# Optimization experiments

Hardware: AMD Instinct MI355X
Metric: run time of the kernel (lower is better)

## Reference

```python
import jax, jax.numpy as jnp
import numpy as np

B, C, H, W = 32, 256, 32, 32
D = max(16, C // 4)  # 64
K = 8


def setup_inputs() -> dict:
    key = jax.random.key(0)
    ks = jax.random.split(key, 4)
    x = jax.random.normal(ks[0], (B, C, H, W), dtype=jnp.float32)
    wq = jax.random.normal(ks[1], (D, C), dtype=jnp.float32) * (1.0 / np.sqrt(C))
    wk = jax.random.normal(ks[2], (D, C), dtype=jnp.float32) * (1.0 / np.sqrt(C))
    wv = jax.random.normal(ks[3], (C, C), dtype=jnp.float32) * (1.0 / np.sqrt(C))
    bq = jnp.zeros((D,), dtype=jnp.float32)
    bk = jnp.zeros((D,), dtype=jnp.float32)
    bv = jnp.zeros((C,), dtype=jnp.float32)
    scale = jnp.ones((1,), dtype=jnp.float32)
    return {"x": x, "wq": wq, "bq": bq, "wk": wk, "bk": bk, "wv": wv, "bv": bv, "scale": scale}


def reference(x, wq, bq, wk, bk, wv, bv, scale):
    b, c, h, w = x.shape
    n = h * w
    xf = x.reshape(b, c, n)                      # [B,C,N]
    # 1x1 convs are pointwise GEMMs over the channel dim
    q = jnp.einsum('dc,bcn->bdn', wq, xf) + bq[None, :, None]   # [B,D,N]
    k = jnp.einsum('dc,bcn->bdn', wk, xf) + bk[None, :, None]   # [B,D,N]
    v = jnp.einsum('ec,bcn->ben', wv, xf) + bv[None, :, None]   # [B,C,N]
    d = q.shape[1]
    sim = jnp.einsum('bdn,bdm->bnm', q, k) / jnp.sqrt(jnp.float32(d))  # [B,N,N]
    sim = sim - 1e9 * jnp.eye(n, dtype=sim.dtype)[None]          # mask self
    topk_val, topk_idx = jax.lax.top_k(sim, K)                    # [B,N,K]
    weights = jax.nn.softmax(topk_val, axis=-1)                   # [B,N,K]
    v_t = v.transpose(0, 2, 1)                                    # [B,N,C]
    gathered = v_t[jnp.arange(b)[:, None, None], topk_idx]        # [B,N,K,C]
    out = jnp.einsum('bnk,bnkc->bnc', weights, gathered)          # [B,N,C]
    out = out.transpose(0, 2, 1).reshape(b, c, h, w)
    return x + scale * out
```

## Files before the change

### kernel.cpp

```cpp
#include <hip/hip_runtime.h>
#include <hip/hip_bf16.h>

#define B_ 32
#define C_ 256
#define N_ 1024
#define D_ 64

typedef __attribute__((ext_vector_type(8))) short bf16x8;
typedef __attribute__((ext_vector_type(4))) float f32x4;

__device__ __forceinline__ unsigned long long pack_key(float v, int m) {
    const unsigned int bits = __float_as_uint(v);
    const unsigned int mono = (bits & 0x80000000u) ? ~bits : (bits | 0x80000000u);
    return ((unsigned long long)mono << 10) | (unsigned long long)(1023 - m);
}

template <int CTRL>
__device__ __forceinline__ float dpp_mov_f(float x) {
    return __int_as_float(__builtin_amdgcn_update_dpp(
        0, __float_as_int(x), CTRL, 0xF, 0xF, true));
}
#define DPP_QUAD_XOR1   0xB1
#define DPP_QUAD_XOR2   0x4E
#define DPP_HALF_MIRROR 0x141
#define DPP_ROW_ROR8    0x128

template <int CTRL>
__device__ __forceinline__ unsigned long long dpp_max_u64(unsigned long long k) {
    const unsigned int lo = (unsigned int)k;
    const unsigned int hi = (unsigned int)(k >> 32);
    const unsigned int plo = (unsigned int)__builtin_amdgcn_update_dpp(0, (int)lo, CTRL, 0xF, 0xF, true);
    const unsigned int phi = (unsigned int)__builtin_amdgcn_update_dpp(0, (int)hi, CTRL, 0xF, 0xF, true);
    const unsigned long long p = ((unsigned long long)phi << 32) | plo;
    return p > k ? p : k;
}

__device__ __forceinline__ unsigned short f2bf(float f) {
    __hip_bfloat16 h = __float2bfloat16(f);
    return *(unsigned short*)&h;
}

__global__ __launch_bounds__(256) void prep_kernel(
    const float* __restrict__ x,
    const float* __restrict__ wq, const float* __restrict__ wk,
    const float* __restrict__ wv, float* __restrict__ wt,
    unsigned short* __restrict__ wvb, unsigned short* __restrict__ xtb,
    int mfma_path)
{
    __shared__ __align__(16) float tl[64][65];
    const int bid = blockIdx.x;
    const int t = threadIdx.x;

    if (bid < 256) {
        const int c = bid;
        for (int r = t; r < 384; r += 256) {
            float v;
            if      (r < 64)  v = wq[(size_t)r * C_ + c];
            else if (r < 128) v = wk[(size_t)(r - 64) * C_ + c];
            else              v = wv[(size_t)(r - 128) * C_ + c];
            wt[(size_t)c * 384 + r] = v;
        }
        if (mfma_path) wvb[(size_t)c * C_ + t] = f2bf(wv[(size_t)c * C_ + t]);
        return;
    }
    if (!mfma_path) return;

    const int lid = bid - 256;
    const int b     = (lid & 7) + 8 * (lid >> 9);
    const int inner = (lid >> 3) & 63;
    const int nt    = inner & 15;
    const int ct    = inner >> 4;
    const int n0 = nt * 64, c0 = ct * 64;

    const float* xb = x + (size_t)b * C_ * N_;
    #pragma unroll
    for (int p = 0; p < 4; ++p) {
        const int cl = (t >> 4) + p * 16;
        const int nl = (t & 15) * 4;
        *(float4*)&tl[cl][nl] = *(const float4*)&xb[(size_t)(c0 + cl) * N_ + n0 + nl];
    }
    __syncthreads();

    unsigned short* dstb = xtb + ((size_t)b * N_) * C_;
    #pragma unroll
    for (int p = 0; p < 4; ++p) {
        const int nl = (t >> 4) + p * 16;
        const int cl = (t & 15) * 4;
        ushort4 o;
        o.x = f2bf(tl[cl + 0][nl]);
        o.y = f2bf(tl[cl + 1][nl]);
        o.z = f2bf(tl[cl + 2][nl]);
        o.w = f2bf(tl[cl + 3][nl]);
        *(ushort4*)&dstb[(size_t)(n0 + nl) * C_ + c0 + cl] = o;
    }
}

__global__ __launch_bounds__(256) void projfused_kernel(
    const float* __restrict__ x, const float* __restrict__ wt,
    const float* __restrict__ bq, const float* __restrict__ bk,
    float* __restrict__ qk,
    const unsigned short* __restrict__ xtb, const unsigned short* __restrict__ wvb,
    const float* __restrict__ bv, float* __restrict__ vt)
{
    const int bid = blockIdx.x;
    const int t = threadIdx.x;
    const int lane = t & 63;

    if (bid < 1024) {
        const int lid = bid;
        const int b     = (lid & 7) + 8 * (lid >> 8);
        const int inner = (lid >> 3) & 31;
        const int rg    = inner & 7;
        const int nt    = inner >> 3;
        const int r0 = rg * 16;
        const int n0 = nt * 256;
        const int wu = __builtin_amdgcn_readfirstlane(t >> 6);
        const int rw = r0 + wu * 4;

        float acc[4][4];
        #pragma unroll
        for (int i = 0; i < 4; ++i)
            #pragma unroll
            for (int j = 0; j < 4; ++j) acc[i][j] = 0.f;

        const float* xp = x + (size_t)b * C_ * N_ + n0 + lane * 4;
        const float* wp = wt + rw;

        #pragma unroll 8
        for (int c = 0; c < C_; ++c) {
            const float4 xv = *(const float4*)(xp + (size_t)c * N_);
            const float4 w0 = *(const float4*)(wp + (size_t)c * 384);
            const float wv4[4] = { w0.x, w0.y, w0.z, w0.w };
            #pragma unroll
            for (int i = 0; i < 4; ++i) {
                acc[i][0] = fmaf(wv4[i], xv.x, acc[i][0]);
                acc[i][1] = fmaf(wv4[i], xv.y, acc[i][1]);
                acc[i][2] = fmaf(wv4[i], xv.z, acc[i][2]);
                acc[i][3] = fmaf(wv4[i], xv.w, acc[i][3]);
            }
        }

        #pragma unroll
        for (int i = 0; i < 4; ++i) {
            const int R = rw + i;
            const float bb = (R < 64) ? bq[R] : bk[R - 64];
            float4 o; o.x = acc[i][0]+bb; o.y = acc[i][1]+bb; o.z = acc[i][2]+bb; o.w = acc[i][3]+bb;
            *(float4*)&qk[((size_t)b * 128 + R) * N_ + n0 + lane * 4] = o;
        }
    } else {
        const int lid = bid - 1024;
        const int b     = (lid & 7) + 8 * (lid >> 9);
        const int inner = (lid >> 3) & 63;
        const int nb    = inner & 15;
        const int eb    = inner >> 4;
        const int w  = t >> 6;
        const int n_base = nb * 64 + (w & 1) * 32;
        const int e_base = eb * 64 + (w >> 1) * 32;

        const int l16  = lane & 15;
        const int koff = 8 * (lane >> 4);

        f32x4 acc[2][2];
        #pragma unroll
        for (int i = 0; i < 2; ++i)
            #pragma unroll
            for (int j = 0; j < 2; ++j) acc[i][j] = (f32x4)(0.f);

        const unsigned short* ab = wvb + (size_t)(e_base + l16) * C_ + koff;
        const unsigned short* bb = xtb + ((size_t)b * N_ + n_base + l16) * C_ + koff;

        #pragma unroll
        for (int kk = 0; kk < 8; ++kk) {
            const int c0 = kk * 32;
            bf16x8 a0 = *(const bf16x8*)(ab + c0);
            bf16x8 a1 = *(const bf16x8*)(ab + 16 * C_ + c0);
            bf16x8 b0 = *(const bf16x8*)(bb + c0);
            bf16x8 b1 = *(const bf16x8*)(bb + 16 * C_ + c0);
            acc[0][0] = __builtin_amdgcn_mfma_f32_16x16x32_bf16(a0, b0, acc[0][0], 0, 0, 0);
            acc[0][1] = __builtin_amdgcn_mfma_f32_16x16x32_bf16(a0, b1, acc[0][1], 0, 0, 0);
            acc[1][0] = __builtin_amdgcn_mfma_f32_16x16x32_bf16(a1, b0, acc[1][0], 0, 0, 0);
            acc[1][1] = __builtin_amdgcn_mfma_f32_16x16x32_bf16(a1, b1, acc[1][1], 0, 0, 0);
        }

        const int col  = lane & 15;
        const int row0 = (lane >> 4) * 4;
        #pragma unroll
        for (int i = 0; i < 2; ++i) {
            const int e0 = e_base + i * 16 + row0;
            const float4 bvv = *(const float4*)&bv[e0];
            #pragma unroll
            for (int j = 0; j < 2; ++j) {
                const int n = n_base + j * 16 + col;
                float4 o;
                o.x = acc[i][j][0] + bvv.x; o.y = acc[i][j][1] + bvv.y;
                o.z = acc[i][j][2] + bvv.z; o.w = acc[i][j][3] + bvv.w;
                *(float4*)&vt[((size_t)b * N_ + n) * C_ + e0] = o;
            }
        }
    }
}

__global__ __launch_bounds__(256) void proj_full_kernel(
    const float* __restrict__ x, const float* __restrict__ wt,
    const float* __restrict__ bq, const float* __restrict__ bk,
    const float* __restrict__ bv,
    float* __restrict__ qk, float* __restrict__ vt)
{
    const int lid = blockIdx.x;
    const int b     = (lid & 7) + 8 * (lid / 384);
    const int inner = (lid >> 3) % 48;
    const int rg    = inner % 12;
    const int nt    = inner / 12;
    const int r0 = rg * 32;
    const int n0 = nt * 256;
    const int lane = threadIdx.x & 63;
    const int wu = __builtin_amdgcn_readfirstlane(threadIdx.x >> 6);
    const int rw = r0 + wu * 8;

    float acc[8][4];
    #pragma unroll
    for (int i = 0; i < 8; ++i)
        #pragma unroll
        for (int j = 0; j < 4; ++j) acc[i][j] = 0.f;

    const float* xp = x + (size_t)b * C_ * N_ + n0 + lane * 4;
    const float* wp = wt + rw;

    #pragma unroll 8
    for (int c = 0; c < C_; ++c) {
        const float4 xv = *(const float4*)(xp + (size_t)c * N_);
        const float* wr = wp + (size_t)c * 384;
        const float4 w0 = *(const float4*)(wr);
        const float4 w1 = *(const float4*)(wr + 4);
        const float wv8[8] = { w0.x, w0.y, w0.z, w0.w, w1.x, w1.y, w1.z, w1.w };
        #pragma unroll
        for (int i = 0; i < 8; ++i) {
            acc[i][0] = fmaf(wv8[i], xv.x, acc[i][0]);
            acc[i][1] = fmaf(wv8[i], xv.y, acc[i][1]);
            acc[i][2] = fmaf(wv8[i], xv.z, acc[i][2]);
            acc[i][3] = fmaf(wv8[i], xv.w, acc[i][3]);
        }
    }

    if (r0 < 128) {
        #pragma unroll
        for (int i = 0; i < 8; ++i) {
            const int R = rw + i;
            const float bb = (R < 64) ? bq[R] : bk[R - 64];
            float4 o; o.x = acc[i][0]+bb; o.y = acc[i][1]+bb; o.z = acc[i][2]+bb; o.w = acc[i][3]+bb;
            *(float4*)&qk[((size_t)b * 128 + R) * N_ + n0 + lane * 4] = o;
        }
    } else {
        const int e0 = rw - 128;
        float be[8];
        #pragma unroll
        for (int i = 0; i < 8; ++i) be[i] = bv[e0 + i];
        #pragma unroll
        for (int j = 0; j < 4; ++j) {
            const int n = n0 + lane * 4 + j;
            float* dst = &vt[((size_t)b * N_ + n) * C_ + e0];
            float4 o0; o0.x = acc[0][j]+be[0]; o0.y = acc[1][j]+be[1]; o0.z = acc[2][j]+be[2]; o0.w = acc[3][j]+be[3];
            float4 o1; o1.x = acc[4][j]+be[4]; o1.y = acc[5][j]+be[5]; o1.z = acc[6][j]+be[6]; o1.w = acc[7][j]+be[7];
            *(float4*)dst       = o0;
            *(float4*)(dst + 4) = o1;
        }
    }
}

__global__ __launch_bounds__(512) void attn_kernel(
    const float* __restrict__ x,
    const float* __restrict__ qk,
    const float* __restrict__ vt,
    const float* __restrict__ scale,
    float* __restrict__ out)
{
    const int lid = blockIdx.x;
    const int b  = (lid & 7) + 8 * (lid >> 9);
    const int n0 = ((lid >> 3) & 63) * 16;
    const int t  = threadIdx.x;
    const int lane = t & 63;
    const int w  = t >> 6;
    const int ms = w & 3;
    const int rg = __builtin_amdgcn_readfirstlane(t >> 8);

    __shared__ unsigned long long cand[16][196];
    __shared__ int   ccnt[16][4];

    const int m_base = ms * 256 + lane * 4;

    float a0[8], a1[8], a2[8], a3[8];
    #pragma unroll
    for (int r = 0; r < 8; ++r) { a0[r]=0.f; a1[r]=0.f; a2[r]=0.f; a3[r]=0.f; }

    const float* kb = qk + ((size_t)b * 128 + 64) * N_ + m_base;
    const float* qb = qk + (size_t)b * 128 * N_ + n0 + rg * 8;

    #pragma unroll 2
    for (int d0 = 0; d0 < D_; d0 += 4) {
        const float4 k0 = *(const float4*)&kb[(size_t)(d0+0) * N_];
        const float4 k1 = *(const float4*)&kb[(size_t)(d0+1) * N_];
        const float4 k2 = *(const float4*)&kb[(size_t)(d0+2) * N_];
        const float4 k3 = *(const float4*)&kb[(size_t)(d0+3) * N_];

        float qs[4][8];
        #pragma unroll
        for (int dd = 0; dd < 4; ++dd) {
            #pragma unroll
            for (int rq = 0; rq < 2; ++rq) {
                const float4 qv = *(const float4*)&qb[(size_t)(d0 + dd) * N_ + rq * 4];
                qs[dd][rq*4+0] = qv.x; qs[dd][rq*4+1] = qv.y;
                qs[dd][rq*4+2] = qv.z; qs[dd][rq*4+3] = qv.w;
            }
        }

        #pragma unroll
        for (int r = 0; r < 8; ++r) {
            a0[r] = fmaf(qs[0][r], k0.x, a0[r]); a0[r] = fmaf(qs[1][r], k1.x, a0[r]);
            a0[r] = fmaf(qs[2][r], k2.x, a0[r]); a0[r] = fmaf(qs[3][r], k3.x, a0[r]);
            a1[r] = fmaf(qs[0][r], k0.y, a1[r]); a1[r] = fmaf(qs[1][r], k1.y, a1[r]);
            a1[r] = fmaf(qs[2][r], k2.y, a1[r]); a1[r] = fmaf(qs[3][r], k3.y, a1[r]);
            a2[r] = fmaf(qs[0][r], k0.z, a2[r]); a2[r] = fmaf(qs[1][r], k1.z, a2[r]);
            a2[r] = fmaf(qs[2][r], k2.z, a2[r]); a2[r] = fmaf(qs[3][r], k3.z, a2[r]);
            a3[r] = fmaf(qs[0][r], k0.w, a3[r]); a3[r] = fmaf(qs[1][r], k1.w, a3[r]);
            a3[r] = fmaf(qs[2][r], k2.w, a3[r]); a3[r] = fmaf(qs[3][r], k3.w, a3[r]);
        }
    }

    const unsigned long long lt = (1ull << lane) - 1ull;
    #pragma unroll
    for (int r = 0; r < 8; ++r) {
        const int ri = rg * 8 + r;
        const int nrow = n0 + ri;
        float t0 = a0[r], t1 = a1[r], t2 = a2[r], t3 = a3[r];
        const int dj = nrow - m_base;
        if      (dj == 0) t0 = -1.0e9f;
        else if (dj == 1) t1 = -1.0e9f;
        else if (dj == 2) t2 = -1.0e9f;
        else if (dj == 3) t3 = -1.0e9f;

        float lm = fmaxf(fmaxf(t0, t1), fmaxf(t2, t3));
        lm = fmaxf(lm, dpp_mov_f<DPP_QUAD_XOR1>(lm));
        lm = fmaxf(lm, dpp_mov_f<DPP_QUAD_XOR2>(lm));
        lm = fmaxf(lm, dpp_mov_f<DPP_HALF_MIRROR>(lm));
        float Th = fminf(lm, dpp_mov_f<DPP_ROW_ROR8>(lm));
        Th = fminf(Th, __shfl_xor(Th, 16));
        Th = fminf(Th, __shfl_xor(Th, 32));

        int cnt = 0;
        {
            const bool p = (t0 >= Th);
            const unsigned long long msk = __ballot(p);
            const int pos = cnt + (int)__popcll(msk & lt);
            if (p && pos < 48) cand[ri][ms * 49 + pos] = pack_key(t0, m_base + 0);
            cnt += (int)__popcll(msk);
        }
        {
            const bool p = (t1 >= Th);
            const unsigned long long msk = __ballot(p);
            const int pos = cnt + (int)__popcll(msk & lt);
            if (p && pos < 48) cand[ri][ms * 49 + pos] = pack_key(t1, m_base + 1);
            cnt += (int)__popcll(msk);
        }
        {
            const bool p = (t2 >= Th);
            const unsigned long long msk = __ballot(p);
            const int pos = cnt + (int)__popcll(msk & lt);
            if (p && pos < 48) cand[ri][ms * 49 + pos] = pack_key(t2, m_base + 2);
            cnt += (int)__popcll(msk);
        }
        {
            const bool p = (t3 >= Th);
            const unsigned long long msk = __ballot(p);
            const int pos = cnt + (int)__popcll(msk & lt);
            if (p && pos < 48) cand[ri][ms * 49 + pos] = pack_key(t3, m_base + 3);
            cnt += (int)__popcll(msk);
        }

        if (cnt > 48) {
            unsigned long long K0 = pack_key(t0, m_base + 0);
            unsigned long long K1 = pack_key(t1, m_base + 1);
            unsigned long long K2 = pack_key(t2, m_base + 2);
            unsigned long long K3 = pack_key(t3, m_base + 3);
            #pragma unroll 1
            for (int round = 0; round < 8; ++round) {
                unsigned long long kl = K0 > K1 ? K0 : K1;
                kl = K2 > kl ? K2 : kl;
                kl = K3 > kl ? K3 : kl;
                #pragma unroll
                for (int off = 32; off >= 1; off >>= 1) {
                    const unsigned long long ks = __shfl_xor(kl, off);
                    if (ks > kl) kl = ks;
                }
                if (lane == 0) cand[ri][ms * 49 + round] = kl;
                if      (K0 == kl) K0 = 0ull;
                else if (K1 == kl) K1 = 0ull;
                else if (K2 == kl) K2 = 0ull;
                else if (K3 == kl) K3 = 0ull;
            }
            cnt = 8;
        }
        if (lane == 0) ccnt[ri][ms] = cnt;
    }
    __syncthreads();

    {
        const int half = lane >> 5;
        const int r    = w * 2 + half;
        const int l5   = lane & 31;

        unsigned long long k[6];
        #pragma unroll
        for (int s = 0; s < 4; ++s)
            k[s] = (l5 < ccnt[r][s]) ? cand[r][s * 49 + l5] : 0ull;
        #pragma unroll
        for (int j = 0; j < 2; ++j) {
            const int g   = l5 + 32 * j;
            const int s   = g >> 4;
            const int pos = 32 + (g & 15);
            k[4 + j] = (pos < ccnt[r][s]) ? cand[r][s * 49 + pos] : 0ull;
        }

        #pragma unroll 1
        for (int round = 0; round < 8; ++round) {
            unsigned long long km = k[0];
            #pragma unroll
            for (int q = 1; q < 6; ++q) km = k[q] > km ? k[q] : km;
            km = dpp_max_u64<DPP_QUAD_XOR1>(km);
            km = dpp_max_u64<DPP_QUAD_XOR2>(km);
            km = dpp_max_u64<DPP_HALF_MIRROR>(km);
            km = dpp_max_u64<DPP_ROW_ROR8>(km);
            { const unsigned long long p = __shfl_xor(km, 16); km = p > km ? p : km; }
            if (l5 == 0) cand[r][188 + round] = km;
            #pragma unroll
            for (int q = 0; q < 6; ++q) if (k[q] == km) k[q] = 0ull;
        }
    }

    const float* vtb = vt + (size_t)b * N_ * C_;
    #pragma unroll 1
    for (int rr = 0; rr < 2; ++rr) {
        const int r = w * 2 + rr;
        float ev[8]; unsigned int mi[8];
        float S = 0.f, vmax = 0.f;
        #pragma unroll
        for (int j = 0; j < 8; ++j) {
            const unsigned long long km = cand[r][188 + j];
            const unsigned int mono = (unsigned int)(km >> 10);
            mi[j] = 1023u - ((unsigned int)km & 1023u);
            const unsigned int bits = (mono & 0x80000000u) ? (mono & 0x7FFFFFFFu) : ~mono;
            const float vraw = __uint_as_float(bits);
            if (j == 0) vmax = vraw;
            const float e = __expf((vraw - vmax) * 0.125f);
            S += e;
            ev[j] = e;
        }

        float4 o = make_float4(0.f, 0.f, 0.f, 0.f);
        #pragma unroll
        for (int j = 0; j < 8; ++j) {
            const float4 vv = *(const float4*)&vtb[(size_t)mi[j] * C_ + lane * 4];
            o.x += ev[j] * vv.x; o.y += ev[j] * vv.y;
            o.z += ev[j] * vv.z; o.w += ev[j] * vv.w;
        }
        const float inv = 1.f / S;
        float* orow = (float*)&cand[r][0];
        *(float4*)&orow[lane * 4] = make_float4(o.x*inv, o.y*inv, o.z*inv, o.w*inv);
    }
    __syncthreads();

    const float sc = scale[0];
    const float* xb = x + (size_t)b * C_ * N_;
    float* ob = out + (size_t)b * C_ * N_;
    const int nl = t & 15;
    const int cg = t >> 4;
    const float* orow = (const float*)&cand[nl][0];
    #pragma unroll
    for (int i = 0; i < 8; ++i) {
        const int cc = i * 32 + cg;
        const size_t gi = (size_t)cc * N_ + n0 + nl;
        ob[gi] = xb[gi] + sc * orow[cc];
    }
}

extern "C" void kernel_launch(void* const* d_in, const int* in_sizes, int n_in,
                              void* d_out, int out_size, void* d_ws, size_t ws_size,
                              hipStream_t stream) {
    const float* x     = (const float*)d_in[0];
    const float* wq    = (const float*)d_in[1];
    const float* bq    = (const float*)d_in[2];
    const float* wk    = (const float*)d_in[3];
    const float* bk    = (const float*)d_in[4];
    const float* wv    = (const float*)d_in[5];
    const float* bv    = (const float*)d_in[6];
    const float* scale = (const float*)d_in[7];
    float* out = (float*)d_out;

    float* qk = (float*)d_ws;
    float* vt = qk + (size_t)B_ * 128 * N_;
    float* wt = vt + (size_t)B_ * N_ * C_;
    unsigned short* wvb = (unsigned short*)(wt + 256 * 384);
    unsigned short* xtb = wvb + (size_t)C_ * C_;

    const size_t needed = ((char*)(xtb + (size_t)B_ * N_ * C_)) - (char*)d_ws;
    const int mfma_path = (ws_size >= needed) ? 1 : 0;

    prep_kernel<<<dim3(256 + 2048), 256, 0, stream>>>(x, wq, wk, wv, wt, wvb, xtb, mfma_path);
    if (mfma_path) {
        projfused_kernel<<<dim3(1024 + 2048), 256, 0, stream>>>(x, wt, bq, bk, qk, xtb, wvb, bv, vt);
    } else {
        proj_full_kernel<<<dim3(1536), 256, 0, stream>>>(x, wt, bq, bk, bv, qk, vt);
    }
    attn_kernel<<<dim3(2048), 512, 0, stream>>>(x, qk, vt, scale, out);
}
```

Baseline: 172.5 us.

## Fuse prep and projection kernels into one launch with in-LDS bf16 transpose

Removes the separate prep kernel, which transposed weights and wrote a bf16 transposed copy of x to global memory. The V-projection blocks now transpose and convert their x tile into shared memory themselves and convert fp32 Wv rows to bf16 on the fly. The Q/K blocks read wq/wk rows directly. This cuts one launch and the global round trip of the bf16 x copy, at the cost of redundant Wv conversion in every block and scalar strided weight loads in the FMA path.

Result: no change. 169.2 us (-2.0%).

```diff
diff --git a/kernel.cpp b/kernel.cpp
--- a/kernel.cpp
+++ b/kernel.cpp
@@ -40,83 +40,119 @@
     return *(unsigned short*)&h;
 }
 
-__global__ __launch_bounds__(256) void prep_kernel(
+__device__ __forceinline__ bf16x8 cvt8(float4 lo, float4 hi) {
+    bf16x8 r;
+    r[0] = (short)f2bf(lo.x); r[1] = (short)f2bf(lo.y);
+    r[2] = (short)f2bf(lo.z); r[3] = (short)f2bf(lo.w);
+    r[4] = (short)f2bf(hi.x); r[5] = (short)f2bf(hi.y);
+    r[6] = (short)f2bf(hi.z); r[7] = (short)f2bf(hi.w);
+    return r;
+}
+
+__global__ __launch_bounds__(512) void projall_kernel(
     const float* __restrict__ x,
-    const float* __restrict__ wq, const float* __restrict__ wk,
-    const float* __restrict__ wv, float* __restrict__ wt,
-    unsigned short* __restrict__ wvb, unsigned short* __restrict__ xtb,
-    int mfma_path)
+    const float* __restrict__ wq, const float* __restrict__ bq,
+    const float* __restrict__ wk, const float* __restrict__ bk,
+    const float* __restrict__ wv, const float* __restrict__ bv,
+    float* __restrict__ qk, float* __restrict__ vt)
 {
     __shared__ __align__(16) float tl[64][65];
-    const int bid = blockIdx.x;
-    const int t = threadIdx.x;
-
-    if (bid < 256) {
-        const int c = bid;
-        for (int r = t; r < 384; r += 256) {
-            float v;
-            if      (r < 64)  v = wq[(size_t)r * C_ + c];
-            else if (r < 128) v = wk[(size_t)(r - 64) * C_ + c];
-            else              v = wv[(size_t)(r - 128) * C_ + c];
-            wt[(size_t)c * 384 + r] = v;
-        }
-        if (mfma_path) wvb[(size_t)c * C_ + t] = f2bf(wv[(size_t)c * C_ + t]);
-        return;
-    }
-    if (!mfma_path) return;
-
-    const int lid = bid - 256;
-    const int b     = (lid & 7) + 8 * (lid >> 9);
-    const int inner = (lid >> 3) & 63;
-    const int nt    = inner & 15;
-    const int ct    = inner >> 4;
-    const int n0 = nt * 64, c0 = ct * 64;
-
-    const float* xb = x + (size_t)b * C_ * N_;
-    #pragma unroll
-    for (int p = 0; p < 4; ++p) {
-        const int cl = (t >> 4) + p * 16;
-        const int nl = (t & 15) * 4;
-        *(float4*)&tl[cl][nl] = *(const float4*)&xb[(size_t)(c0 + cl) * N_ + n0 + nl];
-    }
-    __syncthreads();
-
-    unsigned short* dstb = xtb + ((size_t)b * N_) * C_;
-    #pragma unroll
-    for (int p = 0; p < 4; ++p) {
-        const int nl = (t >> 4) + p * 16;
-        const int cl = (t & 15) * 4;
-        ushort4 o;
-        o.x = f2bf(tl[cl + 0][nl]);
-        o.y = f2bf(tl[cl + 1][nl]);
-        o.z = f2bf(tl[cl + 2][nl]);
-        o.w = f2bf(tl[cl + 3][nl]);
-        *(ushort4*)&dstb[(size_t)(n0 + nl) * C_ + c0 + cl] = o;
-    }
-}
-
-__global__ __launch_bounds__(256) void projfused_kernel(
-    const float* __restrict__ x, const float* __restrict__ wt,
-    const float* __restrict__ bq, const float* __restrict__ bk,
-    float* __restrict__ qk,
-    const unsigned short* __restrict__ xtb, const unsigned short* __restrict__ wvb,
-    const float* __restrict__ bv, float* __restrict__ vt)
-{
+    __shared__ __align__(16) unsigned short xbf[64][264];
+
     const int bid = blockIdx.x;
     const int t = threadIdx.x;
     const int lane = t & 63;
 
-    if (bid < 1024) {
+    if (bid < 512) {
         const int lid = bid;
-        const int b     = (lid & 7) + 8 * (lid >> 8);
-        const int inner = (lid >> 3) & 31;
-        const int rg    = inner & 7;
-        const int nt    = inner >> 3;
+        const int b  = (lid & 7) + 8 * (lid >> 7);
+        const int nb = (lid >> 3) & 15;
+        const int n0 = nb * 64;
+
+        const float* xb = x + (size_t)b * C_ * N_;
+        for (int ct = 0; ct < 4; ++ct) {
+            const int c0 = ct * 64;
+            #pragma unroll
+            for (int p = 0; p < 2; ++p) {
+                const int cl = (t >> 4) + p * 32;
+                const int nl = (t & 15) * 4;
+                *(float4*)&tl[cl][nl] = *(const float4*)&xb[(size_t)(c0 + cl) * N_ + n0 + nl];
+            }
+            __syncthreads();
+            #pragma unroll
+            for (int p = 0; p < 2; ++p) {
+                const int nl = (t >> 4) + p * 32;
+                const int cl4 = (t & 15) * 4;
+                ushort4 o;
+                o.x = f2bf(tl[cl4 + 0][nl]);
+                o.y = f2bf(tl[cl4 + 1][nl]);
+                o.z = f2bf(tl[cl4 + 2][nl]);
+                o.w = f2bf(tl[cl4 + 3][nl]);
+                *(ushort4*)&xbf[nl][c0 + cl4] = o;
+            }
+            __syncthreads();
+        }
+
+        const int w    = t >> 6;
+        const int wn   = w & 1;
+        const int we   = w >> 1;
+        const int l16  = lane & 15;
+        const int koff = 8 * (lane >> 4);
+
+        f32x4 acc[2][4];
+        #pragma unroll
+        for (int i = 0; i < 2; ++i)
+            #pragma unroll
+            for (int j = 0; j < 4; ++j) acc[i][j] = (f32x4)(0.f);
+
+        #pragma unroll
+        for (int kk = 0; kk < 8; ++kk) {
+            const int c0k = kk * 32;
+            const bf16x8 b0 = *(const bf16x8*)&xbf[wn * 32 + l16][koff + c0k];
+            const bf16x8 b1 = *(const bf16x8*)&xbf[wn * 32 + 16 + l16][koff + c0k];
+            #pragma unroll
+            for (int et = 0; et < 4; ++et) {
+                const float* wr = wv + (size_t)(we * 64 + et * 16 + l16) * C_ + koff + c0k;
+                const float4 lo = *(const float4*)wr;
+                const float4 hi = *(const float4*)(wr + 4);
+                const bf16x8 a = cvt8(lo, hi);
+                acc[0][et] = __builtin_amdgcn_mfma_f32_16x16x32_bf16(a, b0, acc[0][et], 0, 0, 0);
+                acc[1][et] = __builtin_amdgcn_mfma_f32_16x16x32_bf16(a, b1, acc[1][et], 0, 0, 0);
+            }
+        }
+
+        const int col  = lane & 15;
+        const int row0 = (lane >> 4) * 4;
+        #pragma unroll
+        for (int et = 0; et < 4; ++et) {
+            const int e0 = we * 64 + et * 16 + row0;
+            const float4 bvv = *(const float4*)&bv[e0];
+            #pragma unroll
+            for (int nt = 0; nt < 2; ++nt) {
+                const int n = n0 + wn * 32 + nt * 16 + col;
+                float4 o;
+                o.x = acc[nt][et][0] + bvv.x; o.y = acc[nt][et][1] + bvv.y;
+                o.z = acc[nt][et][2] + bvv.z; o.w = acc[nt][et][3] + bvv.w;
+                *(float4*)&vt[((size_t)b * N_ + n) * C_ + e0] = o;
+            }
+        }
+    } else {
+        const int lid = bid - 512;
+        const int b   = (lid & 7) + 8 * (lid >> 7);
+        const int rg  = (lid >> 3) & 7;
+        const int ntp = (lid >> 6) & 1;
+        const int sub = __builtin_amdgcn_readfirstlane(t >> 8);
+        const int wu  = __builtin_amdgcn_readfirstlane((t >> 6) & 3);
+        const int nt  = ntp * 2 + sub;
         const int r0 = rg * 16;
         const int n0 = nt * 256;
-        const int wu = __builtin_amdgcn_readfirstlane(t >> 6);
         const int rw = r0 + wu * 4;
 
+        const float* w0p = (rw < 64) ? (wq + (size_t)rw * C_) : (wk + (size_t)(rw - 64) * C_);
+        const float* w1p = w0p + C_;
+        const float* w2p = w0p + 2 * C_;
+        const float* w3p = w0p + 3 * C_;
+
         float acc[4][4];
         #pragma unroll
         for (int i = 0; i < 4; ++i)
@@ -124,13 +160,11 @@
             for (int j = 0; j < 4; ++j) acc[i][j] = 0.f;
 
         const float* xp = x + (size_t)b * C_ * N_ + n0 + lane * 4;
-        const float* wp = wt + rw;
 
         #pragma unroll 8
         for (int c = 0; c < C_; ++c) {
             const float4 xv = *(const float4*)(xp + (size_t)c * N_);
-            const float4 w0 = *(const float4*)(wp + (size_t)c * 384);
-            const float wv4[4] = { w0.x, w0.y, w0.z, w0.w };
+            const float wv4[4] = { w0p[c], w1p[c], w2p[c], w3p[c] };
             #pragma unroll
             for (int i = 0; i < 4; ++i) {
                 acc[i][0] = fmaf(wv4[i], xv.x, acc[i][0]);
@@ -146,123 +180,6 @@
             const float bb = (R < 64) ? bq[R] : bk[R - 64];
             float4 o; o.x = acc[i][0]+bb; o.y = acc[i][1]+bb; o.z = acc[i][2]+bb; o.w = acc[i][3]+bb;
             *(float4*)&qk[((size_t)b * 128 + R) * N_ + n0 + lane * 4] = o;
-        }
-    } else {
-        const int lid = bid - 1024;
-        const int b     = (lid & 7) + 8 * (lid >> 9);
-        const int inner = (lid >> 3) & 63;
-        const int nb    = inner & 15;
-        const int eb    = inner >> 4;
-        const int w  = t >> 6;
-        const int n_base = nb * 64 + (w & 1) * 32;
-        const int e_base = eb * 64 + (w >> 1) * 32;
-
-        const int l16  = lane & 15;
-        const int koff = 8 * (lane >> 4);
-
-        f32x4 acc[2][2];
-        #pragma unroll
-        for (int i = 0; i < 2; ++i)
-            #pragma unroll
-            for (int j = 0; j < 2; ++j) acc[i][j] = (f32x4)(0.f);
-
-        const unsigned short* ab = wvb + (size_t)(e_base + l16) * C_ + koff;
-        const unsigned short* bb = xtb + ((size_t)b * N_ + n_base + l16) * C_ + koff;
-
-        #pragma unroll
-        for (int kk = 0; kk < 8; ++kk) {
-            const int c0 = kk * 32;
-            bf16x8 a0 = *(const bf16x8*)(ab + c0);
-            bf16x8 a1 = *(const bf16x8*)(ab + 16 * C_ + c0);
-            bf16x8 b0 = *(const bf16x8*)(bb + c0);
-            bf16x8 b1 = *(const bf16x8*)(bb + 16 * C_ + c0);
-            acc[0][0] = __builtin_amdgcn_mfma_f32_16x16x32_bf16(a0, b0, acc[0][0], 0, 0, 0);
-            acc[0][1] = __builtin_amdgcn_mfma_f32_16x16x32_bf16(a0, b1, acc[0][1], 0, 0, 0);
-            acc[1][0] = __builtin_amdgcn_mfma_f32_16x16x32_bf16(a1, b0, acc[1][0], 0, 0, 0);
-            acc[1][1] = __builtin_amdgcn_mfma_f32_16x16x32_bf16(a1, b1, acc[1][1], 0, 0, 0);
-        }
-
-        const int col  = lane & 15;
-        const int row0 = (lane >> 4) * 4;
-        #pragma unroll
-        for (int i = 0; i < 2; ++i) {
-            const int e0 = e_base + i * 16 + row0;
-            const float4 bvv = *(const float4*)&bv[e0];
-            #pragma unroll
-            for (int j = 0; j < 2; ++j) {
-                const int n = n_base + j * 16 + col;
-                float4 o;
-                o.x = acc[i][j][0] + bvv.x; o.y = acc[i][j][1] + bvv.y;
-                o.z = acc[i][j][2] + bvv.z; o.w = acc[i][j][3] + bvv.w;
-                *(float4*)&vt[((size_t)b * N_ + n) * C_ + e0] = o;
-            }
-        }
-    }
-}
-
-__global__ __launch_bounds__(256) void proj_full_kernel(
-    const float* __restrict__ x, const float* __restrict__ wt,
-    const float* __restrict__ bq, const float* __restrict__ bk,
-    const float* __restrict__ bv,
-    float* __restrict__ qk, float* __restrict__ vt)
-{
-    const int lid = blockIdx.x;
-    const int b     = (lid & 7) + 8 * (lid / 384);
-    const int inner = (lid >> 3) % 48;
-    const int rg    = inner % 12;
-    const int nt    = inner / 12;
-    const int r0 = rg * 32;
-    const int n0 = nt * 256;
-    const int lane = threadIdx.x & 63;
-    const int wu = __builtin_amdgcn_readfirstlane(threadIdx.x >> 6);
-    const int rw = r0 + wu * 8;
-
-    float acc[8][4];
-    #pragma unroll
-    for (int i = 0; i < 8; ++i)
-        #pragma unroll
-        for (int j = 0; j < 4; ++j) acc[i][j] = 0.f;
-
-    const float* xp = x + (size_t)b * C_ * N_ + n0 + lane * 4;
-    const float* wp = wt + rw;
-
-    #pragma unroll 8
-    for (int c = 0; c < C_; ++c) {
-        const float4 xv = *(const float4*)(xp + (size_t)c * N_);
-        const float* wr = wp + (size_t)c * 384;
-        const float4 w0 = *(const float4*)(wr);
-        const float4 w1 = *(const float4*)(wr + 4);
-        const float wv8[8] = { w0.x, w0.y, w0.z, w0.w, w1.x, w1.y, w1.z, w1.w };
-        #pragma unroll
-        for (int i = 0; i < 8; ++i) {
-            acc[i][0] = fmaf(wv8[i], xv.x, acc[i][0]);
-            acc[i][1] = fmaf(wv8[i], xv.y, acc[i][1]);
-            acc[i][2] = fmaf(wv8[i], xv.z, acc[i][2]);
-            acc[i][3] = fmaf(wv8[i], xv.w, acc[i][3]);
-        }
-    }
-
-    if (r0 < 128) {
-        #pragma unroll
-        for (int i = 0; i < 8; ++i) {
-            const int R = rw + i;
-            const float bb = (R < 64) ? bq[R] : bk[R - 64];
-            float4 o; o.x = acc[i][0]+bb; o.y = acc[i][1]+bb; o.z = acc[i][2]+bb; o.w = acc[i][3]+bb;
-            *(float4*)&qk[((size_t)b * 128 + R) * N_ + n0 + lane * 4] = o;
-        }
-    } else {
-        const int e0 = rw - 128;
-        float be[8];
-        #pragma unroll
-        for (int i = 0; i < 8; ++i) be[i] = bv[e0 + i];
-        #pragma unroll
-        for (int j = 0; j < 4; ++j) {
-            const int n = n0 + lane * 4 + j;
-            float* dst = &vt[((size_t)b * N_ + n) * C_ + e0];
-            float4 o0; o0.x = acc[0][j]+be[0]; o0.y = acc[1][j]+be[1]; o0.z = acc[2][j]+be[2]; o0.w = acc[3][j]+be[3];
-            float4 o1; o1.x = acc[4][j]+be[4]; o1.y = acc[5][j]+be[5]; o1.z = acc[6][j]+be[6]; o1.w = acc[7][j]+be[7];
-            *(float4*)dst       = o0;
-            *(float4*)(dst + 4) = o1;
         }
     }
 }
@@ -497,18 +414,7 @@
 
     float* qk = (float*)d_ws;
     float* vt = qk + (size_t)B_ * 128 * N_;
-    float* wt = vt + (size_t)B_ * N_ * C_;
-    unsigned short* wvb = (unsigned short*)(wt + 256 * 384);
-    unsigned short* xtb = wvb + (size_t)C_ * C_;
-
-    const size_t needed = ((char*)(xtb + (size_t)B_ * N_ * C_)) - (char*)d_ws;
-    const int mfma_path = (ws_size >= needed) ? 1 : 0;
-
-    prep_kernel<<<dim3(256 + 2048), 256, 0, stream>>>(x, wq, wk, wv, wt, wvb, xtb, mfma_path);
-    if (mfma_path) {
-        projfused_kernel<<<dim3(1024 + 2048), 256, 0, stream>>>(x, wt, bq, bk, qk, xtb, wvb, bv, vt);
-    } else {
-        proj_full_kernel<<<dim3(1536), 256, 0, stream>>>(x, wt, bq, bk, bv, qk, vt);
-    }
+
+    projall_kernel<<<dim3(1024), 512, 0, stream>>>(x, wq, bq, wk, bk, wv, bv, qk, vt);
     attn_kernel<<<dim3(2048), 512, 0, stream>>>(x, qk, vt, scale, out);
 }
```
